# Optimization experiments

Measured on AMD Instinct MI355X. Metric: run time of the kernel, lower is better.

The kernel has to match this reference:

```python
import jax, jax.numpy as jnp
import numpy as np

B, W, L = 32768, 5, 20            # batch, words per example, max chars per word
WV, CV = 50000, 100               # word vocab, char vocab
CE, OC, K = 32, 30, 3             # char embed dim, conv out channels (=window_size), kernel
WE, HID, TAGS = 50, 100, 36       # word embed dim, fc1 hidden, output tags


def setup_inputs() -> dict:
    key = jax.random.key(0)
    ks = jax.random.split(key, 8)
    inp = jax.random.randint(ks[0], (B, W, 1 + L), 0, 100, dtype=jnp.int32)
    embedding_matrix = jax.random.normal(ks[1], (WV, WE), jnp.float32).at[0].set(0.0)  # padding_idx=0, frozen
    char_emb = jax.random.normal(ks[2], (CV, CE), jnp.float32).at[0].set(0.0)          # padding_idx=0
    conv_w = jax.random.normal(ks[3], (OC, CE, K), jnp.float32) * 0.1
    conv_b = jnp.zeros((OC,), jnp.float32)
    fc1_w = jax.random.normal(ks[4], (HID, (WE + OC) * W), jnp.float32) * 0.05
    fc1_b = jnp.zeros((HID,), jnp.float32)
    out_w = jax.random.normal(ks[5], (TAGS, HID), jnp.float32) * 0.1
    out_b = jnp.zeros((TAGS,), jnp.float32)
    return dict(input=inp, embedding_matrix=embedding_matrix, char_emb=char_emb,
                conv_w=conv_w, conv_b=conv_b, fc1_w=fc1_w, fc1_b=fc1_b,
                out_w=out_w, out_b=out_b)


def reference(input, embedding_matrix, char_emb, conv_w, conv_b, fc1_w, fc1_b, out_w, out_b):
    b = input.shape[0]
    word_ids = input[:, :, 0]                 # [B, W]
    char_ids = input[:, :, 1:]                # [B, W, L]
    we = embedding_matrix[word_ids]           # [B, W, 50]
    ce = char_emb[char_ids]                   # [B, W, L, CE]
    # conv1d over char axis, batched over all B*W words at once
    x = ce.reshape(b * W, L, CE).transpose(0, 2, 1)        # [B*W, CE, L]
    conv = jax.lax.conv_general_dilated(
        x, conv_w, window_strides=(1,), padding='VALID',
        dimension_numbers=('NCH', 'OIH', 'NCH')) + conv_b[None, :, None]  # [B*W, OC, L-2]
    pooled = conv.max(axis=2).reshape(b, W, OC)            # max pool over time
    feats = jnp.concatenate([we, pooled], axis=-1).reshape(b, -1)  # [B, (50+OC)*W]
    h = jnp.tanh(feats @ fc1_w.T + fc1_b)     # dropout is a no-op at inference
    return h @ out_w.T + out_b                # [B, 36]
```

## Files before the change

kernel.cpp:

```cpp
#include <hip/hip_runtime.h>

#define B_TOT 32768
#define OC 30
#define HID 100
#define TAGS 36

#define WS_TH  0
#define WS_FC1 6000
#define WS_OUT 29296

typedef __attribute__((ext_vector_type(8))) _Float16 half8;
typedef __attribute__((ext_vector_type(2))) _Float16 h2v;
typedef __attribute__((ext_vector_type(4))) float f32x4;

__device__ inline half8 ash8(uint4 u) {
    union { uint4 a; half8 b; } v; v.a = u; return v.b;
}
__device__ inline unsigned int h2u(h2v h) {
    union { h2v a; unsigned int b; } v; v.a = h; return v.b;
}
__device__ inline h2v u2h(unsigned int u) {
    union { unsigned int a; h2v b; } v; v.a = u; return v.b;
}
__device__ inline unsigned int pk_f16(float a, float b) {
    h2v h; h.x = (_Float16)a; h.y = (_Float16)b; return h2u(h);
}

__global__ void prep(const float* __restrict__ conv_w,
                     const float* __restrict__ char_emb,
                     const float* __restrict__ fc1_w,
                     const float* __restrict__ out_w,
                     unsigned int* __restrict__ ws) {
    int idx = blockIdx.x * 256 + threadIdx.x;
    if (idx < 6000) {
        int rd = idx % 20, row = idx / 20;
        int c = row % 100, k = row / 100;
        float v[2];
        #pragma unroll
        for (int e = 0; e < 2; ++e) {
            int oc = rd * 2 + e;
            float s = 0.f;
            if (oc < OC) {
                for (int ce = 0; ce < 32; ++ce)
                    s += char_emb[c * 32 + ce] * conv_w[(oc * 32 + ce) * 3 + k];
            }
            v[e] = s;
        }
        ws[WS_TH + idx] = pk_f16(v[0], v[1]);
    } else if (idx < 6000 + 23296) {
        int t = idx - 6000;
        int dw = t & 3, lane = (t >> 2) & 63, chunk = t >> 8;
        int ks = chunk % 13, nt = chunk / 13;
        int j = nt * 16 + (lane & 15);
        int k = ks * 32 + (lane >> 4) * 8 + dw * 2;
        float a = (j < HID && k     < 400) ? fc1_w[j * 400 + k]     : 0.f;
        float b = (j < HID && k + 1 < 400) ? fc1_w[j * 400 + k + 1] : 0.f;
        ws[WS_FC1 + t] = pk_f16(a, b);
    } else if (idx < 29296 + 3072) {
        int t = idx - 29296;
        int dw = t & 3, lane = (t >> 2) & 63, chunk = t >> 8;
        int ks = chunk % 4, nt = chunk / 4;
        int j = nt * 16 + (lane & 15);
        int k = ks * 32 + (lane >> 4) * 8 + dw * 2;
        float a = (j < TAGS && k     < HID) ? out_w[j * 100 + k]     : 0.f;
        float b = (j < TAGS && k + 1 < HID) ? out_w[j * 100 + k + 1] : 0.f;
        ws[WS_OUT + t] = pk_f16(a, b);
    }
}

__global__ __launch_bounds__(256, 2)
void pos_fused(const int*   __restrict__ input,
               const float* __restrict__ emb,
               const float* __restrict__ conv_b,
               const float* __restrict__ fc1_b,
               const float* __restrict__ out_b,
               const unsigned int* __restrict__ ws,
               float*       __restrict__ out)
{
    __shared__ unsigned int Ths[6000];
    __shared__ unsigned int F[4][16 * 212];

    const int tid  = threadIdx.x;
    const int wv   = tid >> 6;
    const int lane = tid & 63;
    const int ln15 = lane & 15;
    const int quad = lane >> 4;
    const int item0 = blockIdx.x * 64 + wv * 16;
    unsigned int* Fw = &F[wv][0];

    for (int idx = tid; idx < 6000; idx += 256) Ths[idx] = ws[WS_TH + idx];
    __syncthreads();

    {
        int i = lane >> 2, d0 = 200 + (lane & 3) * 2;
        Fw[i * 212 + d0]     = 0;
        Fw[i * 212 + d0 + 1] = 0;
    }

    for (int t = 0; t < 32; ++t) {
        int idx = t * 64 + lane;
        if (idx < 2000) {
            int ph = idx % 25;
            int w  = (idx / 25) % 5;
            int i  = idx / 125;
            int wid = input[(item0 + i) * 105 + w * 21];
            float2 e = *(const float2*)&emb[wid * 50 + ph * 2];
            Fw[i * 212 + w * 40 + ph] = pk_f16(e.x, e.y);
        }
    }

    {
        const int q4  = lane & 3;
        const int grp = lane >> 2;
        const int oc0 = q4 * 8;
        h2v bias[4];
        #pragma unroll
        for (int d = 0; d < 4; ++d) {
            int a = oc0 + 2 * d, b = a + 1;
            bias[d].x = (_Float16)(a < OC ? conv_b[a] : 0.f);
            bias[d].y = (_Float16)(b < OC ? conv_b[b] : 0.f);
        }
        #pragma unroll
        for (int round = 0; round < 5; ++round) {
            int task = round * 16 + grp;
            int i = task / 5, w = task % 5;
            const int* cp = &input[(item0 + i) * 105 + w * 21 + 1];
            int c[20];
            #pragma unroll
            for (int p = 0; p < 20; ++p) c[p] = cp[p];
            h2v m[4];
            #pragma unroll
            for (int d = 0; d < 4; ++d) { m[d].x = (_Float16)(-30000.f); m[d].y = (_Float16)(-30000.f); }
            #pragma unroll 6
            for (int p = 0; p < 18; ++p) {
                uint4 ra = *(const uint4*)&Ths[c[p    ] * 20        + q4 * 4];
                uint4 rb = *(const uint4*)&Ths[c[p + 1] * 20 + 2000 + q4 * 4];
                uint4 rc = *(const uint4*)&Ths[c[p + 2] * 20 + 4000 + q4 * 4];
                unsigned int* pa = (unsigned int*)&ra;
                unsigned int* pb = (unsigned int*)&rb;
                unsigned int* pc = (unsigned int*)&rc;
                #pragma unroll
                for (int d = 0; d < 4; ++d) {
                    h2v s = u2h(pa[d]) + u2h(pb[d]) + u2h(pc[d]);
                    m[d] = __builtin_elementwise_max(m[d], s);
                }
            }
            int base = i * 212 + w * 40 + 25 + q4 * 4;
            Fw[base]     = h2u(m[0] + bias[0]);
            Fw[base + 1] = h2u(m[1] + bias[1]);
            Fw[base + 2] = h2u(m[2] + bias[2]);
            if (q4 < 3) Fw[base + 3] = h2u(m[3] + bias[3]);
        }
    }

    f32x4 acc[7];
    #pragma unroll
    for (int t = 0; t < 7; ++t) acc[t] = f32x4{0, 0, 0, 0};
    {
        const uint4* wp = (const uint4*)(ws + WS_FC1);
        const int aoff = ln15 * 212 + quad * 4;
        for (int ks = 0; ks < 13; ++ks) {
            half8 a = ash8(*(const uint4*)&Fw[aoff + ks * 16]);
            #pragma unroll
            for (int t = 0; t < 7; ++t) {
                uint4 bv = wp[(t * 13 + ks) * 64 + lane];
                acc[t] = __builtin_amdgcn_mfma_f32_16x16x32_f16(a, ash8(bv), acc[t], 0, 0, 0);
            }
        }
    }

    {
        for (int t2 = lane; t2 < 224; t2 += 64) {
            int i = t2 / 14, d = t2 % 14;
            Fw[i * 68 + 50 + d] = 0;
        }
        unsigned short* Hw = (unsigned short*)Fw;
        #pragma unroll
        for (int t = 0; t < 7; ++t) {
            int j = t * 16 + ln15;
            if (j < HID) {
                float bj = fc1_b[j];
                #pragma unroll
                for (int r = 0; r < 4; ++r) {
                    int it = quad * 4 + r;
                    float hv = tanhf(acc[t][r] + bj);
                    _Float16 h = (_Float16)hv;
                    Hw[it * 136 + j] = *reinterpret_cast<unsigned short*>(&h);
                }
            }
        }
    }

    {
        f32x4 oacc[3];
        #pragma unroll
        for (int t = 0; t < 3; ++t) oacc[t] = f32x4{0, 0, 0, 0};
        const uint4* wpo = (const uint4*)(ws + WS_OUT);
        const int aoff2 = ln15 * 68 + quad * 4;
        #pragma unroll
        for (int ks = 0; ks < 4; ++ks) {
            half8 a = ash8(*(const uint4*)&Fw[aoff2 + ks * 16]);
            #pragma unroll
            for (int t = 0; t < 3; ++t) {
                uint4 bv = wpo[(t * 4 + ks) * 64 + lane];
                oacc[t] = __builtin_amdgcn_mfma_f32_16x16x32_f16(a, ash8(bv), oacc[t], 0, 0, 0);
            }
        }
        #pragma unroll
        for (int t = 0; t < 3; ++t) {
            int o = t * 16 + ln15;
            if (o < TAGS) {
                float bo = out_b[o];
                #pragma unroll
                for (int r = 0; r < 4; ++r) {
                    int it = item0 + quad * 4 + r;
                    out[it * TAGS + o] = oacc[t][r] + bo;
                }
            }
        }
    }
}

extern "C" void kernel_launch(void* const* d_in, const int* in_sizes, int n_in,
                              void* d_out, int out_size, void* d_ws, size_t ws_size,
                              hipStream_t stream) {
    const int*   input  = (const int*)  d_in[0];
    const float* emb    = (const float*)d_in[1];
    const float* char_e = (const float*)d_in[2];
    const float* conv_w = (const float*)d_in[3];
    const float* conv_b = (const float*)d_in[4];
    const float* fc1_w  = (const float*)d_in[5];
    const float* fc1_b  = (const float*)d_in[6];
    const float* out_w  = (const float*)d_in[7];
    const float* out_b  = (const float*)d_in[8];
    unsigned int* ws = (unsigned int*)d_ws;

    prep<<<127, 256, 0, stream>>>(conv_w, char_e, fc1_w, out_w, ws);
    pos_fused<<<B_TOT / 64, 256, 0, stream>>>(input, emb, conv_b, fc1_b, out_b,
                                              ws, (float*)d_out);
}
```

Baseline: 127.9 us.

## Split fused kernel into feature-extraction and GEMM kernels via global workspace

Splits the fused kernel into a feature kernel and a GEMM kernel. The feature kernel builds word-embedding and char-conv max-pool features for 16 items per block and stores them as fp16 in global workspace. The GEMM kernel reads them back for the fc1 and output MFMA layers. This frees the large per-wave LDS feature buffer to raise occupancy, at the cost of an extra global round trip of the features and more repeated loads of the conv lookup table per block.

```diff
diff --git a/kernel.cpp b/kernel.cpp
--- a/kernel.cpp
+++ b/kernel.cpp
@@ -8,6 +8,7 @@
 #define WS_TH  0
 #define WS_FC1 6000
 #define WS_OUT 29296
+#define WS_F   40960
 
 typedef __attribute__((ext_vector_type(8))) _Float16 half8;
 typedef __attribute__((ext_vector_type(2))) _Float16 h2v;
@@ -68,50 +69,34 @@
     }
 }
 
-__global__ __launch_bounds__(256, 2)
-void pos_fused(const int*   __restrict__ input,
-               const float* __restrict__ emb,
-               const float* __restrict__ conv_b,
-               const float* __restrict__ fc1_b,
-               const float* __restrict__ out_b,
-               const unsigned int* __restrict__ ws,
-               float*       __restrict__ out)
+__global__ __launch_bounds__(256)
+void feat(const int*   __restrict__ input,
+          const float* __restrict__ emb,
+          const float* __restrict__ conv_b,
+          unsigned int* __restrict__ ws)
 {
     __shared__ unsigned int Ths[6000];
-    __shared__ unsigned int F[4][16 * 212];
-
-    const int tid  = threadIdx.x;
-    const int wv   = tid >> 6;
-    const int lane = tid & 63;
-    const int ln15 = lane & 15;
-    const int quad = lane >> 4;
-    const int item0 = blockIdx.x * 64 + wv * 16;
-    unsigned int* Fw = &F[wv][0];
+
+    const int tid   = threadIdx.x;
+    const int item0 = blockIdx.x * 16;
+    unsigned int* Fg = ws + WS_F;
 
     for (int idx = tid; idx < 6000; idx += 256) Ths[idx] = ws[WS_TH + idx];
     __syncthreads();
 
-    {
-        int i = lane >> 2, d0 = 200 + (lane & 3) * 2;
-        Fw[i * 212 + d0]     = 0;
-        Fw[i * 212 + d0 + 1] = 0;
-    }
-
-    for (int t = 0; t < 32; ++t) {
-        int idx = t * 64 + lane;
-        if (idx < 2000) {
-            int ph = idx % 25;
-            int w  = (idx / 25) % 5;
-            int i  = idx / 125;
-            int wid = input[(item0 + i) * 105 + w * 21];
-            float2 e = *(const float2*)&emb[wid * 50 + ph * 2];
-            Fw[i * 212 + w * 40 + ph] = pk_f16(e.x, e.y);
-        }
-    }
-
-    {
-        const int q4  = lane & 3;
-        const int grp = lane >> 2;
+    if (tid < 128) Fg[(item0 + (tid >> 3)) * 208 + 200 + (tid & 7)] = 0;
+
+    for (int idx = tid; idx < 2000; idx += 256) {
+        int ph = idx % 25;
+        int w  = (idx / 25) % 5;
+        int i  = idx / 125;
+        int wid = input[(item0 + i) * 105 + w * 21];
+        float2 e = *(const float2*)&emb[wid * 50 + ph * 2];
+        Fg[(item0 + i) * 208 + w * 40 + ph] = pk_f16(e.x, e.y);
+    }
+
+    {
+        const int q4  = tid & 3;
         const int oc0 = q4 * 8;
         h2v bias[4];
         #pragma unroll
@@ -120,9 +105,7 @@
             bias[d].x = (_Float16)(a < OC ? conv_b[a] : 0.f);
             bias[d].y = (_Float16)(b < OC ? conv_b[b] : 0.f);
         }
-        #pragma unroll
-        for (int round = 0; round < 5; ++round) {
-            int task = round * 16 + grp;
+        for (int task = tid >> 2; task < 80; task += 64) {
             int i = task / 5, w = task % 5;
             const int* cp = &input[(item0 + i) * 105 + w * 21 + 1];
             int c[20];
@@ -145,22 +128,40 @@
                     m[d] = __builtin_elementwise_max(m[d], s);
                 }
             }
-            int base = i * 212 + w * 40 + 25 + q4 * 4;
-            Fw[base]     = h2u(m[0] + bias[0]);
-            Fw[base + 1] = h2u(m[1] + bias[1]);
-            Fw[base + 2] = h2u(m[2] + bias[2]);
-            if (q4 < 3) Fw[base + 3] = h2u(m[3] + bias[3]);
-        }
-    }
+            int base = (item0 + i) * 208 + w * 40 + 25 + q4 * 4;
+            Fg[base]     = h2u(m[0] + bias[0]);
+            Fg[base + 1] = h2u(m[1] + bias[1]);
+            Fg[base + 2] = h2u(m[2] + bias[2]);
+            if (q4 < 3) Fg[base + 3] = h2u(m[3] + bias[3]);
+        }
+    }
+}
+
+__global__ __launch_bounds__(256)
+void gemm(const float* __restrict__ fc1_b,
+          const float* __restrict__ out_b,
+          const unsigned int* __restrict__ ws,
+          float*       __restrict__ out)
+{
+    __shared__ unsigned int Hh[4][16 * 68];
+
+    const int tid  = threadIdx.x;
+    const int wv   = tid >> 6;
+    const int lane = tid & 63;
+    const int ln15 = lane & 15;
+    const int quad = lane >> 4;
+    const int item0 = blockIdx.x * 64 + wv * 16;
+    unsigned int* Hw = &Hh[wv][0];
+    const unsigned int* Fg = ws + WS_F;
 
     f32x4 acc[7];
     #pragma unroll
     for (int t = 0; t < 7; ++t) acc[t] = f32x4{0, 0, 0, 0};
     {
         const uint4* wp = (const uint4*)(ws + WS_FC1);
-        const int aoff = ln15 * 212 + quad * 4;
+        const unsigned int* arow = Fg + (item0 + ln15) * 208 + quad * 4;
         for (int ks = 0; ks < 13; ++ks) {
-            half8 a = ash8(*(const uint4*)&Fw[aoff + ks * 16]);
+            half8 a = ash8(*(const uint4*)(arow + ks * 16));
             #pragma unroll
             for (int t = 0; t < 7; ++t) {
                 uint4 bv = wp[(t * 13 + ks) * 64 + lane];
@@ -172,9 +173,9 @@
     {
         for (int t2 = lane; t2 < 224; t2 += 64) {
             int i = t2 / 14, d = t2 % 14;
-            Fw[i * 68 + 50 + d] = 0;
-        }
-        unsigned short* Hw = (unsigned short*)Fw;
+            Hw[i * 68 + 50 + d] = 0;
+        }
+        unsigned short* Hs = (unsigned short*)Hw;
         #pragma unroll
         for (int t = 0; t < 7; ++t) {
             int j = t * 16 + ln15;
@@ -185,7 +186,7 @@
                     int it = quad * 4 + r;
                     float hv = tanhf(acc[t][r] + bj);
                     _Float16 h = (_Float16)hv;
-                    Hw[it * 136 + j] = *reinterpret_cast<unsigned short*>(&h);
+                    Hs[it * 136 + j] = *reinterpret_cast<unsigned short*>(&h);
                 }
             }
         }
@@ -196,10 +197,10 @@
         #pragma unroll
         for (int t = 0; t < 3; ++t) oacc[t] = f32x4{0, 0, 0, 0};
         const uint4* wpo = (const uint4*)(ws + WS_OUT);
-        const int aoff2 = ln15 * 68 + quad * 4;
+        const int aoff = ln15 * 68 + quad * 4;
         #pragma unroll
         for (int ks = 0; ks < 4; ++ks) {
-            half8 a = ash8(*(const uint4*)&Fw[aoff2 + ks * 16]);
+            half8 a = ash8(*(const uint4*)&Hw[aoff + ks * 16]);
             #pragma unroll
             for (int t = 0; t < 3; ++t) {
                 uint4 bv = wpo[(t * 4 + ks) * 64 + lane];
@@ -236,6 +237,6 @@
     unsigned int* ws = (unsigned int*)d_ws;
 
     prep<<<127, 256, 0, stream>>>(conv_w, char_e, fc1_w, out_w, ws);
-    pos_fused<<<B_TOT / 64, 256, 0, stream>>>(input, emb, conv_b, fc1_b, out_b,
-                                              ws, (float*)d_out);
-}
+    feat<<<B_TOT / 16, 256, 0, stream>>>(input, emb, conv_b, ws);
+    gemm<<<B_TOT / 64, 256, 0, stream>>>(fc1_b, out_b, ws, (float*)d_out);
+}
```

New measurement: 129.4 us (median of 2 runs). No clear change (+1.1%).
